# Optimization experiments

Hardware: AMD Instinct MI355X
Metric: run time of the kernel (lower is better)

The kernel has to match this reference:

```python
import jax, jax.numpy as jnp
import numpy as np

LOG2 = float(np.log(2.0))
E, G, F, C = 500000, 64, 128, 4

def shifted_softplus(x):
    return jax.nn.softplus(x) - LOG2

def setup_inputs() -> dict:
    key = jax.random.key(0)
    ks = jax.random.split(key, 6)
    return {
        "edge_attr": jax.random.normal(ks[0], (E, G), dtype=jnp.float32),
        "colors": jax.random.randint(ks[1], (E,), 0, C),
        "W1": jax.random.normal(ks[2], (C, G, F), dtype=jnp.float32) * (1.0 / np.sqrt(G)),
        "b1": jax.random.normal(ks[3], (C, F), dtype=jnp.float32) * 0.01,
        "W2": jax.random.normal(ks[4], (C, F, F), dtype=jnp.float32) * (1.0 / np.sqrt(F)),
        "b2": jax.random.normal(ks[5], (C, F), dtype=jnp.float32) * 0.01,
    }

def reference(edge_attr, colors, W1, b1, W2, b2):
    # Apply every color-expert MLP to all edges, then select per-edge expert output.
    # Faithful to the torch loop: out[colors==i] = mlp_i(edge_attr[colors==i]).
    # h: [C, E, F]
    h = jnp.einsum('eg,cgf->cef', edge_attr, W1) + b1[:, None, :]
    h = shifted_softplus(h)
    y = jnp.einsum('cef,cfh->ceh', h, W2) + b2[:, None, :]  # [C, E, F]
    out = y[colors, jnp.arange(E)]  # [E, F] select each edge's own color expert
    return out
```

## Files before the change

kernel.cpp:

```cpp
#include <hip/hip_runtime.h>
#include <hip/hip_bf16.h>

#define G_DIM 64
#define F_DIM 128
#define C_DIM 4
#define NB    512

#define META_COUNTS 0
#define META_BASES  4
#define META_TSTART 9
#define BH_OFF      32
#define IDX_OFF     (32 + NB*C_DIM)

typedef __bf16 bf16x8 __attribute__((ext_vector_type(8)));
typedef float  f32x4  __attribute__((ext_vector_type(4)));

__device__ inline unsigned short f2bf(float f) {
    __bf16 h = (__bf16)f;
    union { __bf16 b; unsigned short u; } v; v.b = h;
    return v.u;
}

__device__ inline float ssp(float x) {
    float t = __expf(-fabsf(x));
    return fmaxf(x, 0.f) + __logf(1.f + t) - 0.69314718055994531f;
}

__global__ void k_prep1(const int* __restrict__ colors, int E, int CH,
                        unsigned* __restrict__ bh,
                        const float* __restrict__ W1, const float* __restrict__ W2,
                        unsigned short* __restrict__ w1t, unsigned short* __restrict__ w2t) {
    int tid = threadIdx.x;
    if (blockIdx.x < NB) {
        __shared__ unsigned h[C_DIM];
        if (tid < C_DIM) h[tid] = 0;
        __syncthreads();
        int lo = blockIdx.x * CH, hi = lo + CH; if (hi > E) hi = E;
        int lane = tid & 63;
        for (int i0 = lo; i0 < hi; i0 += 256) {
            int i = i0 + tid;
            int c = (i < hi) ? colors[i] : -1;
#pragma unroll
            for (int cc = 0; cc < C_DIM; ++cc) {
                unsigned long long m = __ballot(c == cc);
                if (lane == 0 && m) atomicAdd(&h[cc], (unsigned)__popcll(m));
            }
        }
        __syncthreads();
        if (tid < C_DIM) bh[blockIdx.x * C_DIM + tid] = h[tid];
    } else {
        int i = (blockIdx.x - NB) * 256 + tid;
        if (i < C_DIM * F_DIM * G_DIM) {
            int k = i % G_DIM, n = (i / G_DIM) % F_DIM, c = i / (G_DIM * F_DIM);
            w1t[i] = f2bf(W1[(c * G_DIM + k) * F_DIM + n]);
        }
        if (i < C_DIM * F_DIM * F_DIM) {
            int k = i % F_DIM, n = (i / F_DIM) % F_DIM, c = i / (F_DIM * F_DIM);
            w2t[i] = f2bf(W2[(c * F_DIM + k) * F_DIM + n]);
        }
    }
}

__global__ void k_prep2(const int* __restrict__ colors, int E, int CH,
                        const unsigned* __restrict__ bh, unsigned* __restrict__ meta,
                        int* __restrict__ idx) {
    __shared__ unsigned cur[C_DIM], tmpb[C_DIM], tot[C_DIM];
    int tid = threadIdx.x, w = tid >> 6, lane = tid & 63;

    unsigned run = 0;
    for (int b0 = 0; b0 < NB; b0 += 64) {
        int b = b0 + lane;
        unsigned v = bh[b * C_DIM + w];
        unsigned s = v;
#pragma unroll
        for (int d = 1; d < 64; d <<= 1) {
            unsigned t = __shfl_up(s, d, 64);
            if (lane >= d) s += t;
        }
        if (b == (int)blockIdx.x) tmpb[w] = run + s - v;
        run += __shfl(s, 63, 64);
    }
    if (lane == 0) tot[w] = run;
    __syncthreads();
    if (blockIdx.x == 0 && tid == 0) {
        unsigned bsum = 0, tsum = 0;
#pragma unroll
        for (int c = 0; c < C_DIM; ++c) {
            meta[META_BASES + c] = bsum;
            meta[META_COUNTS + c] = tot[c];
            meta[META_TSTART + c] = tsum;
            bsum += tot[c];
            tsum += (tot[c] + 63) >> 6;
        }
        meta[META_BASES + C_DIM] = bsum;
        meta[META_TSTART + C_DIM] = tsum;
    }
    if (lane == 0) {
        unsigned cb = 0;
        for (int c = 0; c < w; ++c) cb += tot[c];
        cur[w] = tmpb[w] + cb;
    }
    __syncthreads();

    int lo = blockIdx.x * CH, hi = lo + CH; if (hi > E) hi = E;
    for (int i0 = lo; i0 < hi; i0 += 256) {
        int i = i0 + tid;
        int c = (i < hi) ? colors[i] : -1;
#pragma unroll
        for (int cc = 0; cc < C_DIM; ++cc) {
            unsigned long long m = __ballot(c == cc);
            if (!m) continue;
            int leader = __ffsll(m) - 1;
            unsigned base = 0;
            if (lane == leader) base = atomicAdd(&cur[cc], (unsigned)__popcll(m));
            base = __shfl(base, leader, 64);
            if (c == cc) {
                unsigned off = __popcll(m & ((1ull << lane) - 1ull));
                idx[base + off] = i;
            }
        }
    }
}

__global__ __launch_bounds__(256, 6) void mlp_main(
    const float* __restrict__ ea, const float* __restrict__ b1,
    const float* __restrict__ b2, const unsigned short* __restrict__ w1t,
    const unsigned short* __restrict__ w2t, const unsigned* __restrict__ meta,
    const int* __restrict__ idx, float* __restrict__ out) {
    __shared__ __align__(16) unsigned short A[64][72];
    __shared__ __align__(16) unsigned short H[64][136];

    unsigned b = blockIdx.x;
    if (b >= meta[META_TSTART + C_DIM]) return;
    int c = 0;
    if (b >= meta[META_TSTART + 1]) c = 1;
    if (b >= meta[META_TSTART + 2]) c = 2;
    if (b >= meta[META_TSTART + 3]) c = 3;
    int t = (int)(b - meta[META_TSTART + c]);
    int segBase = (int)meta[META_BASES + c];
    int segCnt  = (int)meta[META_COUNTS + c];
    int row0 = t * 64;
    int nrows = segCnt - row0; if (nrows > 64) nrows = 64;

    int tid = threadIdx.x, w = tid >> 6, lane = tid & 63;
    int l15 = lane & 15, l4 = lane >> 4;

    int e_all = (lane < nrows) ? idx[segBase + row0 + lane] : -1;

    {
        int e = __shfl(e_all, w * 16 + (lane >> 2), 64);
        int r = w * 16 + (lane >> 2), q = lane & 3;
        unsigned short tmp[16];
        if (e >= 0) {
            const float4* src = (const float4*)(ea + (size_t)e * G_DIM + q * 16);
#pragma unroll
            for (int i = 0; i < 4; ++i) {
                float4 v = src[i];
                tmp[i * 4 + 0] = f2bf(v.x); tmp[i * 4 + 1] = f2bf(v.y);
                tmp[i * 4 + 2] = f2bf(v.z); tmp[i * 4 + 3] = f2bf(v.w);
            }
        } else {
#pragma unroll
            for (int i = 0; i < 16; ++i) tmp[i] = 0;
        }
        *(uint4*)&A[r][q * 16]     = *(uint4*)&tmp[0];
        *(uint4*)&A[r][q * 16 + 8] = *(uint4*)&tmp[8];
    }

    bf16x8 fB1[2][2]; float bias1[2];
#pragma unroll
    for (int nt = 0; nt < 2; ++nt) {
        int n = w * 32 + nt * 16 + l15;
        bias1[nt] = b1[c * F_DIM + n];
#pragma unroll
        for (int ks = 0; ks < 2; ++ks)
            fB1[nt][ks] = *(const bf16x8*)(w1t + ((size_t)(c * F_DIM + n) * G_DIM + ks * 32 + l4 * 8));
    }
    __syncthreads();

    f32x4 acc[4][2];
#pragma unroll
    for (int mt = 0; mt < 4; ++mt)
#pragma unroll
        for (int nt = 0; nt < 2; ++nt) acc[mt][nt] = (f32x4){0.f, 0.f, 0.f, 0.f};
#pragma unroll
    for (int ks = 0; ks < 2; ++ks) {
#pragma unroll
        for (int mt = 0; mt < 4; ++mt) {
            bf16x8 a = *(const bf16x8*)&A[mt * 16 + l15][ks * 32 + l4 * 8];
            acc[mt][0] = __builtin_amdgcn_mfma_f32_16x16x32_bf16(a, fB1[0][ks], acc[mt][0], 0, 0, 0);
            acc[mt][1] = __builtin_amdgcn_mfma_f32_16x16x32_bf16(a, fB1[1][ks], acc[mt][1], 0, 0, 0);
        }
    }

#pragma unroll
    for (int mt = 0; mt < 4; ++mt)
#pragma unroll
        for (int nt = 0; nt < 2; ++nt)
#pragma unroll
            for (int r = 0; r < 4; ++r) {
                float v = acc[mt][nt][r] + bias1[nt];
                H[mt * 16 + l4 * 4 + r][w * 32 + nt * 16 + l15] = f2bf(ssp(v));
            }

    bf16x8 fB2[2][4]; float bias2[2];
#pragma unroll
    for (int nt = 0; nt < 2; ++nt) {
        int n = w * 32 + nt * 16 + l15;
        bias2[nt] = b2[c * F_DIM + n];
#pragma unroll
        for (int ks = 0; ks < 4; ++ks)
            fB2[nt][ks] = *(const bf16x8*)(w2t + ((size_t)(c * F_DIM + n) * F_DIM + ks * 32 + l4 * 8));
    }
    __syncthreads();

#pragma unroll
    for (int mt = 0; mt < 4; ++mt)
#pragma unroll
        for (int nt = 0; nt < 2; ++nt) acc[mt][nt] = (f32x4){0.f, 0.f, 0.f, 0.f};
#pragma unroll
    for (int ks = 0; ks < 4; ++ks) {
#pragma unroll
        for (int mt = 0; mt < 4; ++mt) {
            bf16x8 a = *(const bf16x8*)&H[mt * 16 + l15][ks * 32 + l4 * 8];
            acc[mt][0] = __builtin_amdgcn_mfma_f32_16x16x32_bf16(a, fB2[0][ks], acc[mt][0], 0, 0, 0);
            acc[mt][1] = __builtin_amdgcn_mfma_f32_16x16x32_bf16(a, fB2[1][ks], acc[mt][1], 0, 0, 0);
        }
    }

#pragma unroll
    for (int mt = 0; mt < 4; ++mt) {
#pragma unroll
        for (int r = 0; r < 4; ++r) {
            int e = __shfl(e_all, mt * 16 + l4 * 4 + r, 64);
            if (e >= 0) {
                float* p = out + (size_t)e * F_DIM + w * 32 + l15;
                __builtin_nontemporal_store(acc[mt][0][r] + bias2[0], p);
                __builtin_nontemporal_store(acc[mt][1][r] + bias2[1], p + 16);
            }
        }
    }
}

__global__ void fallback(const float* __restrict__ ea, const int* __restrict__ colors,
                         const float* __restrict__ W1, const float* __restrict__ b1,
                         const float* __restrict__ W2, const float* __restrict__ b2,
                         float* __restrict__ out, int E) {
    __shared__ float sh[4][F_DIM + G_DIM];
    int w = threadIdx.x >> 6, lane = threadIdx.x & 63;
    int e = blockIdx.x * 4 + w;
    bool valid = (e < E);
    int ec = valid ? e : 0;
    int c = colors[ec];
    float* hv = sh[w];
    float* av = sh[w] + F_DIM;
    av[lane] = ea[(size_t)ec * G_DIM + lane];
    __syncthreads();
    for (int f = lane; f < F_DIM; f += 64) {
        float s = b1[c * F_DIM + f];
        for (int g = 0; g < G_DIM; ++g) s += av[g] * W1[(c * G_DIM + g) * F_DIM + f];
        hv[f] = ssp(s);
    }
    __syncthreads();
    for (int f = lane; f < F_DIM; f += 64) {
        float s = b2[c * F_DIM + f];
        for (int k = 0; k < F_DIM; ++k) s += hv[k] * W2[(c * F_DIM + k) * F_DIM + f];
        if (valid) out[(size_t)e * F_DIM + f] = s;
    }
}

extern "C" void kernel_launch(void* const* d_in, const int* in_sizes, int n_in,
                              void* d_out, int out_size, void* d_ws, size_t ws_size,
                              hipStream_t stream) {
    const float* ea     = (const float*)d_in[0];
    const int*   colors = (const int*)d_in[1];
    const float* W1     = (const float*)d_in[2];
    const float* b1     = (const float*)d_in[3];
    const float* W2     = (const float*)d_in[4];
    const float* b2     = (const float*)d_in[5];
    float* out = (float*)d_out;
    int E = in_sizes[1];

    size_t need = (size_t)(IDX_OFF + E) * 4 +
                  (size_t)(C_DIM * F_DIM * G_DIM + C_DIM * F_DIM * F_DIM) * 2;
    if (ws_size < need) {
        int blocks = (E + 3) / 4;
        fallback<<<blocks, 256, 0, stream>>>(ea, colors, W1, b1, W2, b2, out, E);
        return;
    }

    unsigned* meta = (unsigned*)d_ws;
    unsigned* bh   = (unsigned*)d_ws + BH_OFF;
    int* idx = (int*)d_ws + IDX_OFF;
    unsigned short* w1t = (unsigned short*)((char*)d_ws + (size_t)(IDX_OFF + E) * 4);
    unsigned short* w2t = w1t + C_DIM * F_DIM * G_DIM;

    int CH = (E + NB - 1) / NB;
    k_prep1<<<NB + 256, 256, 0, stream>>>(colors, E, CH, bh, W1, W2, w1t, w2t);
    k_prep2<<<NB, 256, 0, stream>>>(colors, E, CH, bh, meta, idx);
    int g = (E + 63) / 64 + C_DIM;
    mlp_main<<<g, 256, 0, stream>>>(ea, b1, b2, w1t, w2t, meta, idx, out);
}
```

Measured before the change: 91.55 us.

## Process four 64-row chunks per block with software-prefetched edge attributes

After: 124.0 us. 35.4% more time.

```diff
diff --git a/kernel.cpp b/kernel.cpp
--- a/kernel.cpp
+++ b/kernel.cpp
@@ -5,6 +5,7 @@
 #define F_DIM 128
 #define C_DIM 4
 #define NB    512
+#define CHUNKS 4
 
 #define META_COUNTS 0
 #define META_BASES  4
@@ -90,7 +91,7 @@
             meta[META_COUNTS + c] = tot[c];
             meta[META_TSTART + c] = tsum;
             bsum += tot[c];
-            tsum += (tot[c] + 63) >> 6;
+            tsum += (tot[c] + 255) >> 8;
         }
         meta[META_BASES + C_DIM] = bsum;
         meta[META_TSTART + C_DIM] = tsum;
@@ -122,7 +123,7 @@
     }
 }
 
-__global__ __launch_bounds__(256, 6) void mlp_main(
+__global__ __launch_bounds__(256, 4) void mlp_main(
     const float* __restrict__ ea, const float* __restrict__ b1,
     const float* __restrict__ b2, const unsigned short* __restrict__ w1t,
     const unsigned short* __restrict__ w2t, const unsigned* __restrict__ meta,
@@ -139,16 +140,36 @@
     int t = (int)(b - meta[META_TSTART + c]);
     int segBase = (int)meta[META_BASES + c];
     int segCnt  = (int)meta[META_COUNTS + c];
-    int row0 = t * 64;
-    int nrows = segCnt - row0; if (nrows > 64) nrows = 64;
+    int srow0 = t * 256;
+    int rem = segCnt - srow0;
 
     int tid = threadIdx.x, w = tid >> 6, lane = tid & 63;
     int l15 = lane & 15, l4 = lane >> 4;
 
-    int e_all = (lane < nrows) ? idx[segBase + row0 + lane] : -1;
+    int e_all[CHUNKS];
+#pragma unroll
+    for (int k = 0; k < CHUNKS; ++k) {
+        int rr = k * 64 + lane;
+        e_all[k] = (rr < rem) ? idx[segBase + srow0 + rr] : -1;
+    }
+
+    bf16x8 fB1[2][2]; float bias1[2];
+    bf16x8 fB2[2][4]; float bias2[2];
+#pragma unroll
+    for (int nt = 0; nt < 2; ++nt) {
+        int n = w * 32 + nt * 16 + l15;
+        bias1[nt] = b1[c * F_DIM + n];
+        bias2[nt] = b2[c * F_DIM + n];
+#pragma unroll
+        for (int ks = 0; ks < 2; ++ks)
+            fB1[nt][ks] = *(const bf16x8*)(w1t + ((size_t)(c * F_DIM + n) * G_DIM + ks * 32 + l4 * 8));
+#pragma unroll
+        for (int ks = 0; ks < 4; ++ks)
+            fB2[nt][ks] = *(const bf16x8*)(w2t + ((size_t)(c * F_DIM + n) * F_DIM + ks * 32 + l4 * 8));
+    }
 
     {
-        int e = __shfl(e_all, w * 16 + (lane >> 2), 64);
+        int e = __shfl(e_all[0], w * 16 + (lane >> 2), 64);
         int r = w * 16 + (lane >> 2), q = lane & 3;
         unsigned short tmp[16];
         if (e >= 0) {
@@ -166,79 +187,91 @@
         *(uint4*)&A[r][q * 16]     = *(uint4*)&tmp[0];
         *(uint4*)&A[r][q * 16 + 8] = *(uint4*)&tmp[8];
     }
-
-    bf16x8 fB1[2][2]; float bias1[2];
-#pragma unroll
-    for (int nt = 0; nt < 2; ++nt) {
-        int n = w * 32 + nt * 16 + l15;
-        bias1[nt] = b1[c * F_DIM + n];
-#pragma unroll
-        for (int ks = 0; ks < 2; ++ks)
-            fB1[nt][ks] = *(const bf16x8*)(w1t + ((size_t)(c * F_DIM + n) * G_DIM + ks * 32 + l4 * 8));
-    }
     __syncthreads();
 
     f32x4 acc[4][2];
 #pragma unroll
-    for (int mt = 0; mt < 4; ++mt)
-#pragma unroll
-        for (int nt = 0; nt < 2; ++nt) acc[mt][nt] = (f32x4){0.f, 0.f, 0.f, 0.f};
-#pragma unroll
-    for (int ks = 0; ks < 2; ++ks) {
+    for (int k = 0; k < CHUNKS; ++k) {
+#pragma unroll
+        for (int mt = 0; mt < 4; ++mt)
+#pragma unroll
+            for (int nt = 0; nt < 2; ++nt) acc[mt][nt] = (f32x4){0.f, 0.f, 0.f, 0.f};
+#pragma unroll
+        for (int ks = 0; ks < 2; ++ks) {
+#pragma unroll
+            for (int mt = 0; mt < 4; ++mt) {
+                bf16x8 a = *(const bf16x8*)&A[mt * 16 + l15][ks * 32 + l4 * 8];
+                acc[mt][0] = __builtin_amdgcn_mfma_f32_16x16x32_bf16(a, fB1[0][ks], acc[mt][0], 0, 0, 0);
+                acc[mt][1] = __builtin_amdgcn_mfma_f32_16x16x32_bf16(a, fB1[1][ks], acc[mt][1], 0, 0, 0);
+            }
+        }
+
+#pragma unroll
+        for (int mt = 0; mt < 4; ++mt)
+#pragma unroll
+            for (int nt = 0; nt < 2; ++nt)
+#pragma unroll
+                for (int r = 0; r < 4; ++r) {
+                    float v = acc[mt][nt][r] + bias1[nt];
+                    H[mt * 16 + l4 * 4 + r][w * 32 + nt * 16 + l15] = f2bf(ssp(v));
+                }
+
+        float4 g0, g1, g2, g3;
+        int en = -1;
+        if (k < CHUNKS - 1) {
+            en = __shfl(e_all[k + 1], w * 16 + (lane >> 2), 64);
+            if (en >= 0) {
+                const float4* src = (const float4*)(ea + (size_t)en * G_DIM + (lane & 3) * 16);
+                g0 = src[0]; g1 = src[1]; g2 = src[2]; g3 = src[3];
+            }
+        }
+        __syncthreads();
+
+#pragma unroll
+        for (int mt = 0; mt < 4; ++mt)
+#pragma unroll
+            for (int nt = 0; nt < 2; ++nt) acc[mt][nt] = (f32x4){0.f, 0.f, 0.f, 0.f};
+#pragma unroll
+        for (int ks = 0; ks < 4; ++ks) {
+#pragma unroll
+            for (int mt = 0; mt < 4; ++mt) {
+                bf16x8 a = *(const bf16x8*)&H[mt * 16 + l15][ks * 32 + l4 * 8];
+                acc[mt][0] = __builtin_amdgcn_mfma_f32_16x16x32_bf16(a, fB2[0][ks], acc[mt][0], 0, 0, 0);
+                acc[mt][1] = __builtin_amdgcn_mfma_f32_16x16x32_bf16(a, fB2[1][ks], acc[mt][1], 0, 0, 0);
+            }
+        }
+
 #pragma unroll
         for (int mt = 0; mt < 4; ++mt) {
-            bf16x8 a = *(const bf16x8*)&A[mt * 16 + l15][ks * 32 + l4 * 8];
-            acc[mt][0] = __builtin_amdgcn_mfma_f32_16x16x32_bf16(a, fB1[0][ks], acc[mt][0], 0, 0, 0);
-            acc[mt][1] = __builtin_amdgcn_mfma_f32_16x16x32_bf16(a, fB1[1][ks], acc[mt][1], 0, 0, 0);
-        }
-    }
-
-#pragma unroll
-    for (int mt = 0; mt < 4; ++mt)
-#pragma unroll
-        for (int nt = 0; nt < 2; ++nt)
 #pragma unroll
             for (int r = 0; r < 4; ++r) {
-                float v = acc[mt][nt][r] + bias1[nt];
-                H[mt * 16 + l4 * 4 + r][w * 32 + nt * 16 + l15] = f2bf(ssp(v));
-            }
-
-    bf16x8 fB2[2][4]; float bias2[2];
-#pragma unroll
-    for (int nt = 0; nt < 2; ++nt) {
-        int n = w * 32 + nt * 16 + l15;
-        bias2[nt] = b2[c * F_DIM + n];
-#pragma unroll
-        for (int ks = 0; ks < 4; ++ks)
-            fB2[nt][ks] = *(const bf16x8*)(w2t + ((size_t)(c * F_DIM + n) * F_DIM + ks * 32 + l4 * 8));
-    }
-    __syncthreads();
-
-#pragma unroll
-    for (int mt = 0; mt < 4; ++mt)
-#pragma unroll
-        for (int nt = 0; nt < 2; ++nt) acc[mt][nt] = (f32x4){0.f, 0.f, 0.f, 0.f};
-#pragma unroll
-    for (int ks = 0; ks < 4; ++ks) {
-#pragma unroll
-        for (int mt = 0; mt < 4; ++mt) {
-            bf16x8 a = *(const bf16x8*)&H[mt * 16 + l15][ks * 32 + l4 * 8];
-            acc[mt][0] = __builtin_amdgcn_mfma_f32_16x16x32_bf16(a, fB2[0][ks], acc[mt][0], 0, 0, 0);
-            acc[mt][1] = __builtin_amdgcn_mfma_f32_16x16x32_bf16(a, fB2[1][ks], acc[mt][1], 0, 0, 0);
-        }
-    }
-
-#pragma unroll
-    for (int mt = 0; mt < 4; ++mt) {
-#pragma unroll
-        for (int r = 0; r < 4; ++r) {
-            int e = __shfl(e_all, mt * 16 + l4 * 4 + r, 64);
-            if (e >= 0) {
-                float* p = out + (size_t)e * F_DIM + w * 32 + l15;
-                __builtin_nontemporal_store(acc[mt][0][r] + bias2[0], p);
-                __builtin_nontemporal_store(acc[mt][1][r] + bias2[1], p + 16);
-            }
-        }
+                int e = __shfl(e_all[k], mt * 16 + l4 * 4 + r, 64);
+                if (e >= 0) {
+                    float* p = out + (size_t)e * F_DIM + w * 32 + l15;
+                    __builtin_nontemporal_store(acc[mt][0][r] + bias2[0], p);
+                    __builtin_nontemporal_store(acc[mt][1][r] + bias2[1], p + 16);
+                }
+            }
+        }
+
+        if (k < CHUNKS - 1) {
+            int r = w * 16 + (lane >> 2), q = lane & 3;
+            unsigned short tmp[16];
+            if (en >= 0) {
+                float4 vv[4] = {g0, g1, g2, g3};
+#pragma unroll
+                for (int i = 0; i < 4; ++i) {
+                    tmp[i * 4 + 0] = f2bf(vv[i].x); tmp[i * 4 + 1] = f2bf(vv[i].y);
+                    tmp[i * 4 + 2] = f2bf(vv[i].z); tmp[i * 4 + 3] = f2bf(vv[i].w);
+                }
+            } else {
+#pragma unroll
+                for (int i = 0; i < 16; ++i) tmp[i] = 0;
+            }
+            *(uint4*)&A[r][q * 16]     = *(uint4*)&tmp[0];
+            *(uint4*)&A[r][q * 16 + 8] = *(uint4*)&tmp[8];
+        }
+        __syncthreads();
     }
 }
 
@@ -298,6 +331,6 @@
     int CH = (E + NB - 1) / NB;
     k_prep1<<<NB + 256, 256, 0, stream>>>(colors, E, CH, bh, W1, W2, w1t, w2t);
     k_prep2<<<NB, 256, 0, stream>>>(colors, E, CH, bh, meta, idx);
-    int g = (E + 63) / 64 + C_DIM;
+    int g = (E + 255) / 256 + C_DIM;
     mlp_main<<<g, 256, 0, stream>>>(ea, b1, b2, w1t, w2t, meta, idx, out);
 }
```
